# Optimization experiments

Hardware: AMD Instinct MI355X
Metric: run time of the kernel (lower is better)

Reference implementation:

```python
import jax, jax.numpy as jnp
import numpy as np


def setup_inputs() -> dict:
    key = jax.random.key(0)
    k1, k2, k3 = jax.random.split(key, 3)
    B, nv = 128, 512
    muTE = jax.random.normal(k1, (B, nv), dtype=jnp.float32)
    covTE = jax.random.normal(k2, (B, nv, nv), dtype=jnp.float32)
    chol = jax.random.normal(k3, (B, nv, nv), dtype=jnp.float32)
    return {"muTE": muTE, "covTE": covTE, "chol": chol}


def reference(muTE, covTE, chol):
    # phi_mat = chol^T @ covTE @ chol   [B, nv, nv]
    nv = chol.shape[-1]
    cholT = jnp.swapaxes(chol, -1, -2)
    phi_mat = jnp.einsum('bij,bjk->bik', cholT, jnp.einsum('bij,bjk->bik', covTE, chol))
    # apply_phi_mat: strict lower triangle kept, diagonal halved, upper zeroed.
    # (the O(n^2) python loop of map_fn in the original is exactly this mask)
    mask = jnp.tril(jnp.ones((nv, nv), dtype=phi_mat.dtype), k=-1) \
           + 0.5 * jnp.eye(nv, dtype=phi_mat.dtype)
    phi_masked = phi_mat * mask  # broadcast over batch
    cholTE = -jnp.einsum('bij,bjk->bik', chol, phi_masked)
    return (muTE, cholTE)
```

## Files before the change

kernel.cpp:

```cpp
#include <hip/hip_runtime.h>
#include <hip/hip_bf16.h>

#define NV 512
#define NB 128
#define NC 64

typedef float fv4 __attribute__((ext_vector_type(4)));
typedef float fv2 __attribute__((ext_vector_type(2)));
typedef float f32x4 __attribute__((ext_vector_type(4)));
typedef short bf8 __attribute__((ext_vector_type(8)));
typedef unsigned short u16x4 __attribute__((ext_vector_type(4)));
typedef unsigned short u16x8 __attribute__((ext_vector_type(8)));
typedef unsigned u32x2 __attribute__((ext_vector_type(2)));
typedef unsigned u32x4 __attribute__((ext_vector_type(4)));

__device__ __forceinline__ unsigned short f2bf(float f) {
  unsigned u = __builtin_bit_cast(unsigned, f);
  u += 0x7fffu + ((u >> 16) & 1u);
  return (unsigned short)(u >> 16);
}

__device__ __forceinline__ unsigned cvt2(float lo, float hi) {
  __hip_bfloat162 h = __float22bfloat162_rn(make_float2(lo, hi));
  unsigned r;
  __builtin_memcpy(&r, &h, sizeof(r));
  return r;
}

__device__ __forceinline__ bf8 pack8(fv4 a0, fv4 a1) {
  u32x4 r;
  r[0] = cvt2(a0[0], a0[1]);
  r[1] = cvt2(a0[2], a0[3]);
  r[2] = cvt2(a1[0], a1[1]);
  r[3] = cvt2(a1[2], a1[3]);
  return __builtin_bit_cast(bf8, r);
}

__device__ __forceinline__ int swzL(int c, int r) {
  return ((c << 10) + (r << 1)) ^ ((c & 7) << 4);
}
__device__ __forceinline__ int swzC(int j, int ii) {
  return ((j << 6) + (ii << 1)) ^ ((j & 3) << 4);
}

__device__ __forceinline__ void gload_lds16(const void* g, void* l) {
  __builtin_amdgcn_global_load_lds(
      (const __attribute__((address_space(1))) unsigned int*)g,
      (__attribute__((address_space(3))) unsigned int*)l, 16, 0, 0);
}

__global__ __launch_bounds__(256, 4)
void convert_LT_kernel(const float* __restrict__ chol,
                       unsigned short* __restrict__ LT) {
  __shared__ unsigned short T[64][72];
  const int bid = blockIdx.x;
  const int b  = bid >> 6;
  const int t  = bid & 63;
  const int ti = t >> 3, tj = t & 7;

  const float* src = chol + ((size_t)b * NV + ti * 64) * NV + tj * 64;
  {
    const int r0 = threadIdx.x >> 4;
    const int c4 = (threadIdx.x & 15) * 4;
    #pragma unroll
    for (int p = 0; p < 4; ++p) {
      const int r = p * 16 + r0;
      fv4 v = *(const fv4*)(src + (size_t)r * NV + c4);
      T[c4 + 0][r] = f2bf(v[0]);
      T[c4 + 1][r] = f2bf(v[1]);
      T[c4 + 2][r] = f2bf(v[2]);
      T[c4 + 3][r] = f2bf(v[3]);
    }
  }
  __syncthreads();
  unsigned short* dst = LT + ((size_t)b * NV + tj * 64) * NV + ti * 64;
  const int c  = threadIdx.x >> 2;
  const int k8 = (threadIdx.x & 3) * 16;
  u16x8 o0, o1;
  #pragma unroll
  for (int q = 0; q < 8; ++q) { o0[q] = T[c][k8 + q]; o1[q] = T[c][k8 + 8 + q]; }
  *(u16x8*)(dst + (size_t)c * NV + k8)     = o0;
  *(u16x8*)(dst + (size_t)c * NV + k8 + 8) = o1;
}


__device__ __forceinline__ void phase_v9_f32(const float* Abase,
                                             const char* H,
                                             f32x4 (&acc0)[4][4], f32x4 (&acc1)[4][4],
                                             int w, int lr, int lq) {
  const float* rA = Abase + (size_t)(w * 64 + lr) * NV + lq * 8;
  #pragma unroll 2
  for (int t = 0; t < 16; ++t) {
    const int kbase = t * 32 + lq * 8;
    bf8 a[4];
    #pragma unroll
    for (int m = 0; m < 4; ++m) {
      fv4 f0 = *(const fv4*)(rA + (size_t)(m * 16) * NV + t * 32);
      fv4 f1 = *(const fv4*)(rA + (size_t)(m * 16) * NV + t * 32 + 4);
      a[m] = pack8(f0, f1);
    }
    bf8 b0[4];
    #pragma unroll
    for (int n = 0; n < 4; ++n)
      b0[n] = *(const bf8*)(H + swzL(n * 16 + lr, kbase));
    #pragma unroll
    for (int m = 0; m < 4; ++m)
      #pragma unroll
      for (int n = 0; n < 4; ++n)
        acc0[m][n] = __builtin_amdgcn_mfma_f32_16x16x32_bf16(a[m], b0[n], acc0[m][n], 0, 0, 0);
    bf8 b1[4];
    #pragma unroll
    for (int n = 0; n < 4; ++n)
      b1[n] = *(const bf8*)(H + swzL(64 + n * 16 + lr, kbase));
    #pragma unroll
    for (int m = 0; m < 4; ++m)
      #pragma unroll
      for (int n = 0; n < 4; ++n)
        acc1[m][n] = __builtin_amdgcn_mfma_f32_16x16x32_bf16(a[m], b1[n], acc1[m][n], 0, 0, 0);
  }
}

__device__ __forceinline__ void phase_v9_bf16(const unsigned short* Abase,
                                              const char* H,
                                              f32x4 (&acc0)[4][4], f32x4 (&acc1)[4][4],
                                              int w, int lr, int lq) {
  const unsigned short* rA = Abase + (size_t)(w * 64 + lr) * NV + lq * 8;
  #pragma unroll 2
  for (int t = 0; t < 16; ++t) {
    const int kbase = t * 32 + lq * 8;
    bf8 a[4];
    #pragma unroll
    for (int m = 0; m < 4; ++m)
      a[m] = *(const bf8*)(rA + (size_t)(m * 16) * NV + t * 32);
    bf8 b0[4];
    #pragma unroll
    for (int n = 0; n < 4; ++n)
      b0[n] = *(const bf8*)(H + swzL(n * 16 + lr, kbase));
    #pragma unroll
    for (int m = 0; m < 4; ++m)
      #pragma unroll
      for (int n = 0; n < 4; ++n)
        acc0[m][n] = __builtin_amdgcn_mfma_f32_16x16x32_bf16(a[m], b0[n], acc0[m][n], 0, 0, 0);
    bf8 b1[4];
    #pragma unroll
    for (int n = 0; n < 4; ++n)
      b1[n] = *(const bf8*)(H + swzL(64 + n * 16 + lr, kbase));
    #pragma unroll
    for (int m = 0; m < 4; ++m)
      #pragma unroll
      for (int n = 0; n < 4; ++n)
        acc1[m][n] = __builtin_amdgcn_mfma_f32_16x16x32_bf16(a[m], b1[n], acc1[m][n], 0, 0, 0);
  }
}

__global__ __launch_bounds__(512, 2)
void fused_cholTE_v9(const float* __restrict__ covTE,
                     const float* __restrict__ chol,
                     const unsigned short* __restrict__ LT,
                     float* __restrict__ out) {
  __shared__ __align__(16) char H[131072];

  const int tid  = threadIdx.x;
  const int w    = tid >> 6;
  const int lane = tid & 63;
  const int lr   = lane & 15;
  const int lq   = lane >> 4;

  const int bid = blockIdx.x;
  const int xcd = bid & 7;
  const int s   = bid >> 3;
  const int b   = xcd * 16 + (s >> 2);
  const int c0  = (s & 3) * 128;

  const float*          Cb  = covTE + (size_t)b * NV * NV;
  const float*          Lb  = chol  + (size_t)b * NV * NV;
  const unsigned short* LTb = LT    + (size_t)b * NV * NV;
  float*                Ob  = out   + (size_t)b * NV * NV;

  f32x4 acc0[4][4], acc1[4][4];

  #pragma unroll
  for (int cc = 0; cc < 16; ++cc) {
    const int c = cc * 8 + w;
    const unsigned short* src = LTb + (size_t)(c0 + c) * NV + ((lane ^ (c & 7)) * 8);
    gload_lds16(src, H + c * 1024);
  }
  asm volatile("s_waitcnt vmcnt(0)" ::: "memory");
  __syncthreads();

  #pragma unroll
  for (int m = 0; m < 4; ++m)
    #pragma unroll
    for (int n = 0; n < 4; ++n) { acc0[m][n] = (f32x4)0.f; acc1[m][n] = (f32x4)0.f; }
  phase_v9_f32(Cb, H, acc0, acc1, w, lr, lq);
  __syncthreads();

  #pragma unroll
  for (int m = 0; m < 4; ++m) {
    #pragma unroll
    for (int n = 0; n < 4; ++n) {
      const int rrow = w * 64 + m * 16 + lq * 4;
      f32x4 a = acc0[m][n];
      u32x2 pk; pk[0] = cvt2(a[0], a[1]); pk[1] = cvt2(a[2], a[3]);
      *(u32x2*)(H + swzL(n * 16 + lr, rrow)) = pk;
      a = acc1[m][n];
      pk[0] = cvt2(a[0], a[1]); pk[1] = cvt2(a[2], a[3]);
      *(u32x2*)(H + swzL(64 + n * 16 + lr, rrow)) = pk;
    }
  }
  __syncthreads();

  #pragma unroll
  for (int m = 0; m < 4; ++m)
    #pragma unroll
    for (int n = 0; n < 4; ++n) { acc0[m][n] = (f32x4)0.f; acc1[m][n] = (f32x4)0.f; }
  phase_v9_bf16(LTb, H, acc0, acc1, w, lr, lq);
  __syncthreads();

  #pragma unroll
  for (int jt = 0; jt < 4; ++jt) {
    #pragma unroll
    for (int n = 0; n < 4; ++n) {
      const int j0 = w * 64 + jt * 16 + lq * 4;
      const int gk0 = c0 + n * 16 + lr;
      const int gk1 = gk0 + 64;
      f32x4 a = acc0[jt][n];
      float f[4];
      #pragma unroll
      for (int q = 0; q < 4; ++q) {
        const int j = j0 + q;
        f[q] = (j > gk0) ? a[q] : ((j == gk0) ? 0.5f * a[q] : 0.f);
      }
      u32x2 pk; pk[0] = cvt2(f[0], f[1]); pk[1] = cvt2(f[2], f[3]);
      *(u32x2*)(H + swzL(n * 16 + lr, j0)) = pk;
      a = acc1[jt][n];
      #pragma unroll
      for (int q = 0; q < 4; ++q) {
        const int j = j0 + q;
        f[q] = (j > gk1) ? a[q] : ((j == gk1) ? 0.5f * a[q] : 0.f);
      }
      pk[0] = cvt2(f[0], f[1]); pk[1] = cvt2(f[2], f[3]);
      *(u32x2*)(H + swzL(64 + n * 16 + lr, j0)) = pk;
    }
  }
  __syncthreads();

  #pragma unroll
  for (int m = 0; m < 4; ++m)
    #pragma unroll
    for (int n = 0; n < 4; ++n) { acc0[m][n] = (f32x4)0.f; acc1[m][n] = (f32x4)0.f; }
  phase_v9_f32(Lb, H, acc0, acc1, w, lr, lq);

  #pragma unroll
  for (int m = 0; m < 4; ++m) {
    const int i0 = w * 64 + m * 16 + lq * 4;
    #pragma unroll
    for (int n = 0; n < 4; ++n) {
      const int col = c0 + n * 16 + lr;
      f32x4 a = acc0[m][n];
      #pragma unroll
      for (int q = 0; q < 4; ++q)
        Ob[(size_t)(i0 + q) * NV + col] = -a[q];
      a = acc1[m][n];
      #pragma unroll
      for (int q = 0; q < 4; ++q)
        Ob[(size_t)(i0 + q) * NV + col + 64] = -a[q];
    }
  }
}

__global__ __launch_bounds__(1024, 1)
void fused_cholTE_fallback(const float* __restrict__ covTE,
                           const float* __restrict__ chol,
                           float* __restrict__ out) {
  __shared__ __align__(16) char lds[131072];
  char* sB0 = lds;
  char* sB1 = lds + 65536;
  char* sCh = lds;

  const int tid  = threadIdx.x;
  const int w    = tid >> 6;
  const int lane = tid & 63;
  const int lr   = lane & 15;
  const int lq   = lane >> 4;

  const int bid = blockIdx.x;
  const int xcd = bid & 7;
  const int s   = bid >> 3;
  const int b   = xcd * 16 + (s >> 3);
  const int c0  = (s & 7) * NC;

  const float* Cb = covTE + (size_t)b * NV * NV;
  const float* Lb = chol  + (size_t)b * NV * NV;
  float*       Ob = out   + (size_t)b * NV * NV;

  {
    const int rr = tid >> 4;
    const int cc = (tid & 15) * 4;
    #pragma unroll
    for (int p = 0; p < 8; ++p) {
      const int r = p * 64 + rr;
      fv4 v = *(const fv4*)(Lb + (size_t)r * NV + c0 + cc);
      *(unsigned short*)(sB0 + swzL(cc + 0, r)) = f2bf(v[0]);
      *(unsigned short*)(sB0 + swzL(cc + 1, r)) = f2bf(v[1]);
      *(unsigned short*)(sB0 + swzL(cc + 2, r)) = f2bf(v[2]);
      *(unsigned short*)(sB0 + swzL(cc + 3, r)) = f2bf(v[3]);
    }
  }
  __syncthreads();

  f32x4 acc[2][4];
  #pragma unroll
  for (int m = 0; m < 2; ++m)
    #pragma unroll
    for (int n = 0; n < 4; ++n) acc[m][n] = (f32x4)0.f;

  for (int kb = 0; kb < 16; ++kb) {
    const int kbase = kb * 32 + lq * 8;
    bf8 bfr[4];
    #pragma unroll
    for (int n = 0; n < 4; ++n)
      bfr[n] = *(const bf8*)(sB0 + swzL(n * 16 + lr, kbase));
    #pragma unroll
    for (int m = 0; m < 2; ++m) {
      const float* p = Cb + (size_t)(w * 32 + m * 16 + lr) * NV + kbase;
      fv4 a0 = *(const fv4*)p;
      fv4 a1 = *(const fv4*)(p + 4);
      bf8 af = pack8(a0, a1);
      #pragma unroll
      for (int n = 0; n < 4; ++n)
        acc[m][n] = __builtin_amdgcn_mfma_f32_16x16x32_bf16(af, bfr[n], acc[m][n], 0, 0, 0);
    }
  }
  #pragma unroll
  for (int m = 0; m < 2; ++m) {
    #pragma unroll
    for (int n = 0; n < 4; ++n) {
      f32x4 a = acc[m][n];
      u32x2 pk; pk[0] = cvt2(a[0], a[1]); pk[1] = cvt2(a[2], a[3]);
      *(u32x2*)(sB1 + swzL(n * 16 + lr, w * 32 + m * 16 + lq * 4)) = pk;
    }
  }
  __syncthreads();

  #pragma unroll
  for (int m = 0; m < 2; ++m)
    #pragma unroll
    for (int n = 0; n < 4; ++n) acc[m][n] = (f32x4)0.f;

  const int sj = (tid & 255) * 2;
  const int so = tid >> 8;

  fv2 raw[8];
  {
    const float* src = Lb + (size_t)(so * 8) * NV + sj;
    #pragma unroll
    for (int r = 0; r < 8; ++r) raw[r] = *(const fv2*)(src + (size_t)r * NV);
    u16x8 p0, p1;
    #pragma unroll
    for (int r = 0; r < 8; ++r) { p0[r] = f2bf(raw[r][0]); p1[r] = f2bf(raw[r][1]); }
    *(u16x8*)(sCh + swzC(sj + 0, so * 8)) = p0;
    *(u16x8*)(sCh + swzC(sj + 1, so * 8)) = p1;
  }
  __syncthreads();

  for (int ib = 0; ib < 16; ++ib) {
    if (ib + 1 < 16) {
      const float* src = Lb + (size_t)((ib + 1) * 32 + so * 8) * NV + sj;
      #pragma unroll
      for (int r = 0; r < 8; ++r) raw[r] = *(const fv2*)(src + (size_t)r * NV);
    }
    bf8 bt[4];
    #pragma unroll
    for (int n = 0; n < 4; ++n)
      bt[n] = *(const bf8*)(sB1 + swzL(n * 16 + lr, ib * 32 + lq * 8));
    #pragma unroll
    for (int jt = 0; jt < 2; ++jt) {
      bf8 af = *(const bf8*)(sCh + swzC(w * 32 + jt * 16 + lr, lq * 8));
      #pragma unroll
      for (int n = 0; n < 4; ++n)
        acc[jt][n] = __builtin_amdgcn_mfma_f32_16x16x32_bf16(af, bt[n], acc[jt][n], 0, 0, 0);
    }
    __syncthreads();
    if (ib + 1 < 16) {
      u16x8 p0, p1;
      #pragma unroll
      for (int r = 0; r < 8; ++r) { p0[r] = f2bf(raw[r][0]); p1[r] = f2bf(raw[r][1]); }
      *(u16x8*)(sCh + swzC(sj + 0, so * 8)) = p0;
      *(u16x8*)(sCh + swzC(sj + 1, so * 8)) = p1;
    }
    __syncthreads();
  }

  #pragma unroll
  for (int jt = 0; jt < 2; ++jt) {
    #pragma unroll
    for (int n = 0; n < 4; ++n) {
      f32x4 a = acc[jt][n];
      const int gk = c0 + n * 16 + lr;
      const int j0 = w * 32 + jt * 16 + lq * 4;
      float f[4];
      #pragma unroll
      for (int q = 0; q < 4; ++q) {
        const int j = j0 + q;
        f[q] = (j > gk) ? a[q] : ((j == gk) ? 0.5f * a[q] : 0.f);
      }
      u32x2 pk; pk[0] = cvt2(f[0], f[1]); pk[1] = cvt2(f[2], f[3]);
      *(u32x2*)(sB0 + swzL(n * 16 + lr, j0)) = pk;
    }
  }
  __syncthreads();

  #pragma unroll
  for (int m = 0; m < 2; ++m)
    #pragma unroll
    for (int n = 0; n < 4; ++n) acc[m][n] = (f32x4)0.f;

  for (int kb = 0; kb < 16; ++kb) {
    const int kbase = kb * 32 + lq * 8;
    bf8 bp[4];
    #pragma unroll
    for (int n = 0; n < 4; ++n)
      bp[n] = *(const bf8*)(sB0 + swzL(n * 16 + lr, kbase));
    #pragma unroll
    for (int m = 0; m < 2; ++m) {
      const float* p = Lb + (size_t)(w * 32 + m * 16 + lr) * NV + kbase;
      fv4 a0 = *(const fv4*)p;
      fv4 a1 = *(const fv4*)(p + 4);
      bf8 af = pack8(a0, a1);
      #pragma unroll
      for (int n = 0; n < 4; ++n)
        acc[m][n] = __builtin_amdgcn_mfma_f32_16x16x32_bf16(af, bp[n], acc[m][n], 0, 0, 0);
    }
  }
  #pragma unroll
  for (int m = 0; m < 2; ++m) {
    const int i0 = w * 32 + m * 16 + lq * 4;
    #pragma unroll
    for (int n = 0; n < 4; ++n) {
      f32x4 a = acc[m][n];
      const int col = c0 + n * 16 + lr;
      #pragma unroll
      for (int q = 0; q < 4; ++q)
        Ob[(size_t)(i0 + q) * NV + col] = -a[q];
    }
  }
}

extern "C" void kernel_launch(void* const* d_in, const int* in_sizes, int n_in,
                              void* d_out, int out_size, void* d_ws, size_t ws_size,
                              hipStream_t stream) {
  const float* muTE  = (const float*)d_in[0];
  const float* covTE = (const float*)d_in[1];
  const float* chol  = (const float*)d_in[2];
  float* out = (float*)d_out;

  (void)hipMemcpyAsync(out, muTE, (size_t)NB * NV * sizeof(float),
                       hipMemcpyDeviceToDevice, stream);

  float* cholTE = out + (size_t)NB * NV;
  const size_t nmat     = (size_t)NB * NV * NV;
  const size_t lt_bytes = nmat * sizeof(unsigned short);

  if (ws_size >= lt_bytes) {
    unsigned short* LT = (unsigned short*)d_ws;
    convert_LT_kernel<<<dim3(NB * 64), dim3(256), 0, stream>>>(chol, LT);
    fused_cholTE_v9<<<dim3(NB * 4), dim3(512), 0, stream>>>(covTE, chol, LT, cholTE);
  } else {
    fused_cholTE_fallback<<<dim3(NB * (NV / NC)), dim3(1024), 0, stream>>>(
        covTE, chol, cholTE);
  }
}
```

Measured before the change: 239.1 us.

## Pre-convert covTE and chol to bf16 and stream A tiles via LDS loads

Adds a pass that converts covTE to bf16 and has the LT transpose kernel also write a row-major bf16 copy of chol. A new fused kernel then reads bf16 operands instead of fp32, staging A tiles into per-wave LDS buffers with global_load_lds, which replaces the in-loop fp32 loads and packing. Operand bytes inside the main kernel are halved, at the cost of an extra conversion pass over covTE and a larger workspace requirement (three bf16 matrices). If the workspace is too small, the code falls back to the old path.

```diff
diff --git a/kernel.cpp b/kernel.cpp
--- a/kernel.cpp
+++ b/kernel.cpp
@@ -50,8 +50,20 @@
 }
 
 __global__ __launch_bounds__(256, 4)
+void conv_f32_bf16_kernel(const float* __restrict__ src, unsigned short* __restrict__ dst) {
+  const size_t i8 = ((size_t)blockIdx.x * 256 + threadIdx.x) * 8;
+  fv4 a0 = *(const fv4*)(src + i8);
+  fv4 a1 = *(const fv4*)(src + i8 + 4);
+  u32x4 r;
+  r[0] = cvt2(a0[0], a0[1]); r[1] = cvt2(a0[2], a0[3]);
+  r[2] = cvt2(a1[0], a1[1]); r[3] = cvt2(a1[2], a1[3]);
+  *(u32x4*)(dst + i8) = r;
+}
+
+__global__ __launch_bounds__(256, 4)
 void convert_LT_kernel(const float* __restrict__ chol,
-                       unsigned short* __restrict__ LT) {
+                       unsigned short* __restrict__ LT,
+                       unsigned short* __restrict__ LR) {
   __shared__ unsigned short T[64][72];
   const int bid = blockIdx.x;
   const int b  = bid >> 6;
@@ -70,6 +82,10 @@
       T[c4 + 1][r] = f2bf(v[1]);
       T[c4 + 2][r] = f2bf(v[2]);
       T[c4 + 3][r] = f2bf(v[3]);
+      if (LR) {
+        u32x2 pk; pk[0] = cvt2(v[0], v[1]); pk[1] = cvt2(v[2], v[3]);
+        *(u32x2*)(LR + ((size_t)b * NV + ti * 64 + r) * NV + tj * 64 + c4) = pk;
+      }
     }
   }
   __syncthreads();
@@ -83,6 +99,169 @@
   *(u16x8*)(dst + (size_t)c * NV + k8 + 8) = o1;
 }
 
+__device__ __forceinline__ void stageA10(const unsigned short* A, int t, char* buf,
+                                         int w, int lane) {
+  const int row = lane >> 2;
+  const int ko  = (lane & 3) * 8;
+  #pragma unroll
+  for (int pi = 0; pi < 4; ++pi) {
+    const unsigned short* src = A + (size_t)(w * 64 + pi * 16 + row) * NV + t * 32 + ko;
+    gload_lds16(src, buf + pi * 1024);
+  }
+}
+
+__device__ __forceinline__ void phase_v10(const unsigned short* Abase,
+                                          const char* H, char* buf,
+                                          f32x4 (&acc0)[4][4], f32x4 (&acc1)[4][4],
+                                          int w, int lane, int lr, int lq) {
+  stageA10(Abase, 0, buf, w, lane);
+  #pragma unroll 2
+  for (int t = 0; t < 16; ++t) {
+    const int kbase = t * 32 + lq * 8;
+    asm volatile("s_waitcnt vmcnt(0)" ::: "memory");
+    bf8 a[4];
+    #pragma unroll
+    for (int m = 0; m < 4; ++m)
+      a[m] = *(const bf8*)(buf + (m * 16 + lr) * 64 + lq * 16);
+    if (t + 1 < 16) stageA10(Abase, t + 1, buf, w, lane);
+    bf8 b0[4];
+    #pragma unroll
+    for (int n = 0; n < 4; ++n)
+      b0[n] = *(const bf8*)(H + swzL(n * 16 + lr, kbase));
+    #pragma unroll
+    for (int m = 0; m < 4; ++m)
+      #pragma unroll
+      for (int n = 0; n < 4; ++n)
+        acc0[m][n] = __builtin_amdgcn_mfma_f32_16x16x32_bf16(a[m], b0[n], acc0[m][n], 0, 0, 0);
+    bf8 b1[4];
+    #pragma unroll
+    for (int n = 0; n < 4; ++n)
+      b1[n] = *(const bf8*)(H + swzL(64 + n * 16 + lr, kbase));
+    #pragma unroll
+    for (int m = 0; m < 4; ++m)
+      #pragma unroll
+      for (int n = 0; n < 4; ++n)
+        acc1[m][n] = __builtin_amdgcn_mfma_f32_16x16x32_bf16(a[m], b1[n], acc1[m][n], 0, 0, 0);
+  }
+}
+
+__global__ __launch_bounds__(512, 2)
+void fused_cholTE_v10(const unsigned short* __restrict__ CV,
+                      const unsigned short* __restrict__ LR,
+                      const unsigned short* __restrict__ LT,
+                      float* __restrict__ out) {
+  __shared__ __align__(16) char lds[163840];
+  char* H = lds;
+
+  const int tid  = threadIdx.x;
+  const int w    = tid >> 6;
+  const int lane = tid & 63;
+  const int lr   = lane & 15;
+  const int lq   = lane >> 4;
+  char* buf = lds + 131072 + w * 4096;
+
+  const int bid = blockIdx.x;
+  const int xcd = bid & 7;
+  const int s   = bid >> 3;
+  const int b   = xcd * 16 + (s >> 2);
+  const int c0  = (s & 3) * 128;
+
+  const unsigned short* CVb = CV + (size_t)b * NV * NV;
+  const unsigned short* LRb = LR + (size_t)b * NV * NV;
+  const unsigned short* LTb = LT + (size_t)b * NV * NV;
+  float*                Ob  = out + (size_t)b * NV * NV;
+
+  f32x4 acc0[4][4], acc1[4][4];
+
+  #pragma unroll
+  for (int cc = 0; cc < 16; ++cc) {
+    const int c = cc * 8 + w;
+    const unsigned short* src = LTb + (size_t)(c0 + c) * NV + ((lane ^ (c & 7)) * 8);
+    gload_lds16(src, H + c * 1024);
+  }
+  asm volatile("s_waitcnt vmcnt(0)" ::: "memory");
+  __syncthreads();
+
+  #pragma unroll
+  for (int m = 0; m < 4; ++m)
+    #pragma unroll
+    for (int n = 0; n < 4; ++n) { acc0[m][n] = (f32x4)0.f; acc1[m][n] = (f32x4)0.f; }
+  phase_v10(CVb, H, buf, acc0, acc1, w, lane, lr, lq);
+  __syncthreads();
+
+  #pragma unroll
+  for (int m = 0; m < 4; ++m) {
+    #pragma unroll
+    for (int n = 0; n < 4; ++n) {
+      const int rrow = w * 64 + m * 16 + lq * 4;
+      f32x4 a = acc0[m][n];
+      u32x2 pk; pk[0] = cvt2(a[0], a[1]); pk[1] = cvt2(a[2], a[3]);
+      *(u32x2*)(H + swzL(n * 16 + lr, rrow)) = pk;
+      a = acc1[m][n];
+      pk[0] = cvt2(a[0], a[1]); pk[1] = cvt2(a[2], a[3]);
+      *(u32x2*)(H + swzL(64 + n * 16 + lr, rrow)) = pk;
+    }
+  }
+  __syncthreads();
+
+  #pragma unroll
+  for (int m = 0; m < 4; ++m)
+    #pragma unroll
+    for (int n = 0; n < 4; ++n) { acc0[m][n] = (f32x4)0.f; acc1[m][n] = (f32x4)0.f; }
+  phase_v10(LTb, H, buf, acc0, acc1, w, lane, lr, lq);
+  __syncthreads();
+
+  #pragma unroll
+  for (int jt = 0; jt < 4; ++jt) {
+    #pragma unroll
+    for (int n = 0; n < 4; ++n) {
+      const int j0 = w * 64 + jt * 16 + lq * 4;
+      const int gk0 = c0 + n * 16 + lr;
+      const int gk1 = gk0 + 64;
+      f32x4 a = acc0[jt][n];
+      float f[4];
+      #pragma unroll
+      for (int q = 0; q < 4; ++q) {
+        const int j = j0 + q;
+        f[q] = (j > gk0) ? a[q] : ((j == gk0) ? 0.5f * a[q] : 0.f);
+      }
+      u32x2 pk; pk[0] = cvt2(f[0], f[1]); pk[1] = cvt2(f[2], f[3]);
+      *(u32x2*)(H + swzL(n * 16 + lr, j0)) = pk;
+      a = acc1[jt][n];
+      #pragma unroll
+      for (int q = 0; q < 4; ++q) {
+        const int j = j0 + q;
+        f[q] = (j > gk1) ? a[q] : ((j == gk1) ? 0.5f * a[q] : 0.f);
+      }
+      pk[0] = cvt2(f[0], f[1]); pk[1] = cvt2(f[2], f[3]);
+      *(u32x2*)(H + swzL(64 + n * 16 + lr, j0)) = pk;
+    }
+  }
+  __syncthreads();
+
+  #pragma unroll
+  for (int m = 0; m < 4; ++m)
+    #pragma unroll
+    for (int n = 0; n < 4; ++n) { acc0[m][n] = (f32x4)0.f; acc1[m][n] = (f32x4)0.f; }
+  phase_v10(LRb, H, buf, acc0, acc1, w, lane, lr, lq);
+
+  #pragma unroll
+  for (int m = 0; m < 4; ++m) {
+    const int i0 = w * 64 + m * 16 + lq * 4;
+    #pragma unroll
+    for (int n = 0; n < 4; ++n) {
+      const int col = c0 + n * 16 + lr;
+      f32x4 a = acc0[m][n];
+      #pragma unroll
+      for (int q = 0; q < 4; ++q)
+        Ob[(size_t)(i0 + q) * NV + col] = -a[q];
+      a = acc1[m][n];
+      #pragma unroll
+      for (int q = 0; q < 4; ++q)
+        Ob[(size_t)(i0 + q) * NV + col + 64] = -a[q];
+    }
+  }
+}
 
 __device__ __forceinline__ void phase_v9_f32(const float* Abase,
                                              const char* H,
@@ -462,9 +641,16 @@
   const size_t nmat     = (size_t)NB * NV * NV;
   const size_t lt_bytes = nmat * sizeof(unsigned short);
 
-  if (ws_size >= lt_bytes) {
+  if (ws_size >= 3 * lt_bytes) {
+    unsigned short* CV = (unsigned short*)d_ws;
+    unsigned short* LR = CV + nmat;
+    unsigned short* LT = LR + nmat;
+    conv_f32_bf16_kernel<<<dim3(nmat / (256 * 8)), dim3(256), 0, stream>>>(covTE, CV);
+    convert_LT_kernel<<<dim3(NB * 64), dim3(256), 0, stream>>>(chol, LT, LR);
+    fused_cholTE_v10<<<dim3(NB * 4), dim3(512), 0, stream>>>(CV, LR, LT, cholTE);
+  } else if (ws_size >= lt_bytes) {
     unsigned short* LT = (unsigned short*)d_ws;
-    convert_LT_kernel<<<dim3(NB * 64), dim3(256), 0, stream>>>(chol, LT);
+    convert_LT_kernel<<<dim3(NB * 64), dim3(256), 0, stream>>>(chol, LT, nullptr);
     fused_cholTE_v9<<<dim3(NB * 4), dim3(512), 0, stream>>>(covTE, chol, LT, cholTE);
   } else {
     fused_cholTE_fallback<<<dim3(NB * (NV / NC)), dim3(1024), 0, stream>>>(
```

After: 212.1 us. -11.3%, faster.
